# Kernel optimization log

Measured on AMD Instinct MI355X. Metric: run time of the kernel, lower is better.

## Reference

```python
import jax, jax.numpy as jnp
import numpy as np

D_MODEL = 256
NHEAD = 8
NUM_EXPERTS = 5
LQ, LK, BATCH = 100, 1024, 16
LN_EPS = 1e-5


def setup_inputs() -> dict:
    key = jax.random.key(0)
    ks = jax.random.split(key, 12)
    d, E = D_MODEL, NUM_EXPERTS
    s = 1.0 / np.sqrt(d)
    return {
        "tgt": jax.random.normal(ks[0], (LQ, BATCH, d), jnp.float32),
        "memory": jax.random.normal(ks[1], (LK, BATCH, d), jnp.float32),
        "query_pos": jax.random.normal(ks[2], (LQ, BATCH, d), jnp.float32),
        "pos": jax.random.normal(ks[3], (LK, BATCH, d), jnp.float32),
        # per-expert MultiheadAttention params (packed q,k,v in_proj like torch)
        "w_in": jax.random.normal(ks[4], (E, 3 * d, d), jnp.float32) * s,
        "b_in": jnp.zeros((E, 3 * d), jnp.float32),
        "w_out": jax.random.normal(ks[5], (E, d, d), jnp.float32) * s,
        "b_out": jnp.zeros((E, d), jnp.float32),
        # gating network
        "w_gate": jax.random.normal(ks[6], (E, d), jnp.float32) * s,
        "b_gate": jnp.zeros((E,), jnp.float32),
        # LayerNorm
        "ln_gamma": jnp.ones((d,), jnp.float32),
        "ln_beta": jnp.zeros((d,), jnp.float32),
    }


def _moe_cross_attn(tgt, memory, query_pos, pos, w_in, b_in, w_out, b_out,
                    w_gate, b_gate, ln_gamma, ln_beta):
    Lq, B, d = tgt.shape
    H = NHEAD
    hd = d // H
    E = w_in.shape[0]
    Lk = memory.shape[0]

    # gating over (seq*batch, d) -> softmax over experts
    gate = jax.nn.softmax(tgt @ w_gate.T + b_gate, axis=-1)  # (Lq, B, E)

    q_emb = tgt + query_pos      # (Lq, B, d)
    k_emb = memory + pos         # (Lk, B, d)

    wq, wk, wv = w_in[:, :d], w_in[:, d:2 * d], w_in[:, 2 * d:]
    bq, bk, bv = b_in[:, :d], b_in[:, d:2 * d], b_in[:, 2 * d:]

    # batched projections across all experts (replaces python loop of MHA calls)
    q = jnp.einsum('lbd,eod->elbo', q_emb, wq) + bq[:, None, None, :]
    k = jnp.einsum('sbd,eod->esbo', k_emb, wk) + bk[:, None, None, :]
    v = jnp.einsum('sbd,eod->esbo', memory, wv) + bv[:, None, None, :]

    q = q.reshape(E, Lq, B, H, hd) * (1.0 / np.sqrt(hd))
    k = k.reshape(E, Lk, B, H, hd)
    v = v.reshape(E, Lk, B, H, hd)

    scores = jnp.einsum('elbhk,esbhk->ebhls', q, k)      # (E, B, H, Lq, Lk)
    attn = jax.nn.softmax(scores, axis=-1)
    ctx = jnp.einsum('ebhls,esbhk->elbhk', attn, v).reshape(E, Lq, B, d)

    out = jnp.einsum('elbd,eod->elbo', ctx, w_out) + b_out[:, None, None, :]

    # softmax-gated weighted combine of expert outputs
    mo = jnp.einsum('lbe,elbd->lbd', gate, out)

    x = tgt + mo  # dropout is identity (p=0.0)
    mu = jnp.mean(x, axis=-1, keepdims=True)
    var = jnp.var(x, axis=-1, keepdims=True)
    return (x - mu) * jax.lax.rsqrt(var + LN_EPS) * ln_gamma + ln_beta


def reference(tgt, memory, query_pos, pos, w_in, b_in, w_out, b_out,
              w_gate, b_gate, ln_gamma, ln_beta):
    return _moe_cross_attn(tgt, memory, query_pos, pos, w_in, b_in, w_out,
                           b_out, w_gate, b_gate, ln_gamma, ln_beta)
```

## Files before the change

kernel.cpp:

```cpp
#include <hip/hip_runtime.h>


typedef __bf16 bf16x8 __attribute__((ext_vector_type(8)));
typedef float f32x4 __attribute__((ext_vector_type(4)));
typedef unsigned int u32x4 __attribute__((ext_vector_type(4)));
typedef unsigned int u32x2 __attribute__((ext_vector_type(2)));
typedef unsigned short u16x4 __attribute__((ext_vector_type(4)));
typedef unsigned short us;

__device__ __forceinline__ us f2bf(float f) {
    unsigned u = __builtin_bit_cast(unsigned, f);
    u += 0x7FFFu + ((u >> 16) & 1u);
    return (us)(u >> 16);
}

__device__ __forceinline__ float bf2f(us v) {
    unsigned u = ((unsigned)v) << 16;
    return __builtin_bit_cast(float, u);
}

__device__ __forceinline__ bf16x8 ld_bf8(const us* p) {
    return __builtin_bit_cast(bf16x8, *reinterpret_cast<const u32x4*>(p));
}

__device__ __forceinline__ void gld_lds16(const us* g, us* l) {
    __builtin_amdgcn_global_load_lds(
        (const __attribute__((address_space(1))) unsigned int*)g,
        (__attribute__((address_space(3))) unsigned int*)l, 16, 0, 0);
}

__launch_bounds__(256)
__global__ void cvt_all(const float* __restrict__ tgt, const float* __restrict__ qpos,
                        const float* __restrict__ mem, const float* __restrict__ pos,
                        const float* __restrict__ w_in, const float* __restrict__ w_out,
                        us* __restrict__ Aq, us* __restrict__ Ak, us* __restrict__ Av,
                        us* __restrict__ Wb, us* __restrict__ WOb)
{
    const int bid = blockIdx.x;
    const int tid = threadIdx.x;
    if (bid < 400) {
        int i = bid * 256 + tid;
        f32x4 a = reinterpret_cast<const f32x4*>(tgt)[i];
        f32x4 b = reinterpret_cast<const f32x4*>(qpos)[i];
        u16x4 r;
#pragma unroll
        for (int j = 0; j < 4; ++j) r[j] = f2bf(a[j] + b[j]);
        reinterpret_cast<u16x4*>(Aq)[i] = r;
    } else if (bid < 4496) {
        int i = (bid - 400) * 256 + tid;
        f32x4 m = reinterpret_cast<const f32x4*>(mem)[i];
        f32x4 p = reinterpret_cast<const f32x4*>(pos)[i];
        u16x4 rk, rv;
#pragma unroll
        for (int j = 0; j < 4; ++j) { rk[j] = f2bf(m[j] + p[j]); rv[j] = f2bf(m[j]); }
        reinterpret_cast<u16x4*>(Ak)[i] = rk;
        reinterpret_cast<u16x4*>(Av)[i] = rv;
    } else if (bid < 5456) {
        int i = (bid - 4496) * 256 + tid;
        f32x4 a = reinterpret_cast<const f32x4*>(w_in)[i];
        u16x4 r;
#pragma unroll
        for (int j = 0; j < 4; ++j) r[j] = f2bf(a[j]);
        reinterpret_cast<u16x4*>(Wb)[i] = r;
    } else {
        int i = (bid - 5456) * 256 + tid;
        f32x4 a = reinterpret_cast<const f32x4*>(w_out)[i];
        u16x4 r;
#pragma unroll
        for (int j = 0; j < 4; ++j) r[j] = f2bf(a[j]);
        reinterpret_cast<u16x4*>(WOb)[i] = r;
    }
}

template <bool BF16OUT>
__device__ __forceinline__ void gemm_body(const us* __restrict__ A,
                                          const us* __restrict__ W,
                                          const float* __restrict__ bias,
                                          void* __restrict__ Cout,
                                          float scale, int M)
{
    const int row0 = blockIdx.x * 128;
    const int col0 = blockIdx.y * 128;
    __shared__ us As[2 * 8192];
    __shared__ us Bs[2 * 8192];
    const int tid  = threadIdx.x;
    const int lane = tid & 63;
    const int w    = tid >> 6;
    const int l15  = lane & 15;
    const int quad = lane >> 4;
    const int wm   = (w >> 1) * 64;
    const int wn   = (w & 1) * 64;
    const int srow = lane >> 3;
    const int gofs = ((lane & 7) ^ srow) * 8;

#pragma unroll
    for (int cc = 0; cc < 4; ++cc) {
        const int c = w * 4 + cc;
        const int row = c * 8 + srow;
        gld_lds16(A + (size_t)(row0 + row) * 256 + gofs, &As[c * 512]);
        gld_lds16(W + (size_t)(col0 + row) * 256 + gofs, &Bs[c * 512]);
    }
    __syncthreads();

    f32x4 acc[4][4] = {};

#pragma unroll
    for (int kt = 0; kt < 4; ++kt) {
        const int cur = (kt & 1) * 8192;
        if (kt < 3) {
            const int nxt = ((kt + 1) & 1) * 8192;
            const int k0 = (kt + 1) * 64;
#pragma unroll
            for (int cc = 0; cc < 4; ++cc) {
                const int c = w * 4 + cc;
                const int row = c * 8 + srow;
                gld_lds16(A + (size_t)(row0 + row) * 256 + k0 + gofs, &As[nxt + c * 512]);
                gld_lds16(W + (size_t)(col0 + row) * 256 + k0 + gofs, &Bs[nxt + c * 512]);
            }
        }
#pragma unroll
        for (int kh = 0; kh < 2; ++kh) {
            bf16x8 af[4], bf[4];
#pragma unroll
            for (int mi = 0; mi < 4; ++mi) {
                const int row = wm + mi * 16 + l15;
                const int seg = (kh * 4 + quad) ^ (row & 7);
                af[mi] = ld_bf8(&As[cur + row * 64 + seg * 8]);
            }
#pragma unroll
            for (int ni = 0; ni < 4; ++ni) {
                const int col = wn + ni * 16 + l15;
                const int seg = (kh * 4 + quad) ^ (col & 7);
                bf[ni] = ld_bf8(&Bs[cur + col * 64 + seg * 8]);
            }
#pragma unroll
            for (int mi = 0; mi < 4; ++mi)
#pragma unroll
                for (int ni = 0; ni < 4; ++ni)
                    acc[mi][ni] = __builtin_amdgcn_mfma_f32_16x16x32_bf16(bf[ni], af[mi], acc[mi][ni], 0, 0, 0);
        }
        if (kt < 3) __syncthreads();
    }

#pragma unroll
    for (int ni = 0; ni < 4; ++ni) {
        const int colb = col0 + wn + ni * 16 + quad * 4;
        const f32x4 b4 = *reinterpret_cast<const f32x4*>(bias + colb);
#pragma unroll
        for (int mi = 0; mi < 4; ++mi) {
            const int row = row0 + wm + mi * 16 + l15;
            if (row < M) {
                if constexpr (BF16OUT) {
                    u32x2 pk;
                    pk[0] = (unsigned)f2bf((acc[mi][ni][0] + b4[0]) * scale)
                          | ((unsigned)f2bf((acc[mi][ni][1] + b4[1]) * scale) << 16);
                    pk[1] = (unsigned)f2bf((acc[mi][ni][2] + b4[2]) * scale)
                          | ((unsigned)f2bf((acc[mi][ni][3] + b4[3]) * scale) << 16);
                    *reinterpret_cast<u32x2*>(reinterpret_cast<us*>(Cout) + (size_t)row * 256 + colb) = pk;
                } else {
                    f32x4 v;
#pragma unroll
                    for (int r = 0; r < 4; ++r) v[r] = (acc[mi][ni][r] + b4[r]) * scale;
                    *reinterpret_cast<f32x4*>(reinterpret_cast<float*>(Cout) + (size_t)row * 256 + colb) = v;
                }
            }
        }
    }
}

__launch_bounds__(256)
__global__ void gemm_qkv(const us* __restrict__ Aq, const us* __restrict__ Ak,
                         const us* __restrict__ Av, const us* __restrict__ Wb,
                         const float* __restrict__ b_in,
                         us* __restrict__ Qb, us* __restrict__ Kb, us* __restrict__ Vb)
{
    const int z = blockIdx.z;
    if (z < 5) {
        if (blockIdx.x >= 13) return;
        gemm_body<true>(Aq, Wb + (size_t)z * 196608, b_in + (size_t)z * 768,
                        Qb + (size_t)z * 409600, 0.17677669529663687f, 1600);
    } else if (z < 10) {
        const int e = z - 5;
        gemm_body<true>(Ak, Wb + 65536 + (size_t)e * 196608, b_in + (size_t)e * 768 + 256,
                        Kb + (size_t)e * 4194304, 1.0f, 16384);
    } else {
        const int e = z - 10;
        gemm_body<true>(Av, Wb + 131072 + (size_t)e * 196608, b_in + (size_t)e * 768 + 512,
                        Vb + (size_t)e * 4194304, 1.0f, 16384);
    }
}

__launch_bounds__(256)
__global__ void gemm_o(const us* __restrict__ CTXb, const us* __restrict__ WOb,
                       const float* __restrict__ b_out, float* __restrict__ OUTf)
{
    const int e = blockIdx.z;
    gemm_body<false>(CTXb + (size_t)e * 409600, WOb + (size_t)e * 65536,
                     b_out + (size_t)e * 256, OUTf + (size_t)e * 409600, 1.0f, 1600);
}

__device__ __forceinline__ int vrow(int d) { return d * 264 + 8 * (d >> 3); }

__launch_bounds__(512)
__global__ void attn(const us* __restrict__ Qb, const us* __restrict__ Kb,
                     const us* __restrict__ Vb, us* __restrict__ PO,
                     float* __restrict__ PL)
{
    const int h = blockIdx.x;
    const int z = blockIdx.y;
    const int s = blockIdx.z;
    const int e = z >> 4, b = z & 15;
    const int tid  = threadIdx.x;
    const int w    = tid >> 6;
    const int lane = tid & 63;
    const int l15  = lane & 15, quad = lane >> 4;
    __shared__ us Ks[256 * 32];
    __shared__ us Vs[8464];
    __shared__ us Ps[7][16 * 40];

    const int key0 = s * 256;
    {
        const int kl  = lane >> 2;
        const int seg = lane & 3;
        const us* kg = Kb + ((size_t)((e * 1024 + key0 + w * 16 + kl) * 16 + b)) * 256
                          + h * 32 + seg * 8;
        gld_lds16(kg, &Ks[w * 512]);
        gld_lds16(kg + (size_t)128 * 16 * 256, &Ks[4096 + w * 512]);

        const int kv = tid >> 2;
        const int sg = tid & 3;
        const us* vg = Vb + ((size_t)((e * 1024 + key0 + kv) * 16 + b)) * 256
                          + h * 32 + sg * 8;
        u32x4 v0 = *reinterpret_cast<const u32x4*>(vg);
        u32x4 v1 = *reinterpret_cast<const u32x4*>(vg + (size_t)128 * 16 * 256);
#pragma unroll
        for (int j = 0; j < 4; ++j) {
            const int d0 = sg * 8 + 2 * j;
            const int e0 = vrow(d0);
            const int e1 = e0 + 264;
            Vs[e0 + kv]       = (us)(v0[j] & 0xffff);
            Vs[e1 + kv]       = (us)(v0[j] >> 16);
            Vs[e0 + 128 + kv] = (us)(v1[j] & 0xffff);
            Vs[e1 + 128 + kv] = (us)(v1[j] >> 16);
        }
    }
    u32x4 qraw = {0u, 0u, 0u, 0u};
    if (w < 7) {
        const int l = w * 16 + l15;
        if (l < 100)
            qraw = *reinterpret_cast<const u32x4*>(
                Qb + ((size_t)((e * 100 + l) * 16 + b)) * 256 + h * 32 + quad * 8);
    }
    const bf16x8 qf = __builtin_bit_cast(bf16x8, qraw);

    __syncthreads();

    if (w >= 7) return;

    const f32x4 zacc = {};
    f32x4 o0 = {}, o1 = {};
    float lsum = 0.0f;

    for (int c = 0; c < 8; ++c) {
        bf16x8 kf0 = ld_bf8(&Ks[(c * 32 + l15) * 32 + quad * 8]);
        bf16x8 kf1 = ld_bf8(&Ks[(c * 32 + 16 + l15) * 32 + quad * 8]);
        f32x4 s0 = __builtin_amdgcn_mfma_f32_16x16x32_bf16(kf0, qf, zacc, 0, 0, 0);
        f32x4 s1 = __builtin_amdgcn_mfma_f32_16x16x32_bf16(kf1, qf, zacc, 0, 0, 0);
        float p0[4], p1[4];
#pragma unroll
        for (int r = 0; r < 4; ++r) {
            p0[r] = __expf(s0[r]);
            p1[r] = __expf(s1[r]);
            lsum += p0[r] + p1[r];
        }
        u32x2 w0, w1;
        w0[0] = (unsigned)f2bf(p0[0]) | ((unsigned)f2bf(p0[1]) << 16);
        w0[1] = (unsigned)f2bf(p0[2]) | ((unsigned)f2bf(p0[3]) << 16);
        w1[0] = (unsigned)f2bf(p1[0]) | ((unsigned)f2bf(p1[1]) << 16);
        w1[1] = (unsigned)f2bf(p1[2]) | ((unsigned)f2bf(p1[3]) << 16);
        *reinterpret_cast<u32x2*>(&Ps[w][l15 * 40 + quad * 4])      = w0;
        *reinterpret_cast<u32x2*>(&Ps[w][l15 * 40 + 16 + quad * 4]) = w1;
        bf16x8 pf  = ld_bf8(&Ps[w][l15 * 40 + quad * 8]);
        bf16x8 vf0 = ld_bf8(&Vs[vrow(l15) + c * 32 + quad * 8]);
        bf16x8 vf1 = ld_bf8(&Vs[vrow(16 + l15) + c * 32 + quad * 8]);
        o0 = __builtin_amdgcn_mfma_f32_16x16x32_bf16(pf, vf0, o0, 0, 0, 0);
        o1 = __builtin_amdgcn_mfma_f32_16x16x32_bf16(pf, vf1, o1, 0, 0, 0);
    }

    lsum += __shfl_xor(lsum, 16, 64);
    lsum += __shfl_xor(lsum, 32, 64);

#pragma unroll
    for (int r = 0; r < 4; ++r) {
        const int row = w * 16 + quad * 4 + r;
        if (row < 100) {
            const size_t o = (((size_t)((s * 5 + e) * 100 + row)) * 16 + b) * 256 + h * 32;
            PO[o + l15]      = f2bf(o0[r]);
            PO[o + 16 + l15] = f2bf(o1[r]);
        }
    }
    const int q = w * 16 + l15;
    if (quad == 0 && q < 100)
        PL[((((size_t)s * 5 + e) * 16 + b) * 8 + h) * 128 + q] = lsum;
}

__launch_bounds__(256)
__global__ void combine(const us* __restrict__ PO, const float* __restrict__ PL,
                        us* __restrict__ CTX)
{
    const int blk = blockIdx.x;
    const int e   = blk / 1600;
    const int rem = blk - e * 1600;
    const int row = rem >> 4;
    const int b   = rem & 15;
    const int d   = threadIdx.x;
    const int h   = d >> 5;
    float O = 0.0f, L = 0.0f;
#pragma unroll
    for (int s = 0; s < 4; ++s) {
        O += bf2f(PO[(((size_t)((s * 5 + e) * 100 + row)) * 16 + b) * 256 + d]);
        L += PL[((((size_t)s * 5 + e) * 16 + b) * 8 + h) * 128 + row];
    }
    CTX[(((size_t)(e * 100 + row)) * 16 + b) * 256 + d] = f2bf(O / L);
}

__launch_bounds__(256)
__global__ void finalize(const float* __restrict__ tgt, const float* __restrict__ w_gate,
                         const float* __restrict__ b_gate, const float* __restrict__ OUTf,
                         const float* __restrict__ gamma, const float* __restrict__ beta,
                         float* __restrict__ out)
{
    const int row = blockIdx.x;
    const int d = threadIdx.x;
    __shared__ float red[4];
    const float t = tgt[(size_t)row * 256 + d];

    float g[5];
#pragma unroll
    for (int e = 0; e < 5; ++e) {
        float part = t * w_gate[e * 256 + d];
#pragma unroll
        for (int off = 32; off >= 1; off >>= 1) part += __shfl_xor(part, off, 64);
        if ((d & 63) == 0) red[d >> 6] = part;
        __syncthreads();
        g[e] = red[0] + red[1] + red[2] + red[3] + b_gate[e];
        __syncthreads();
    }
    float mx = g[0];
#pragma unroll
    for (int e = 1; e < 5; ++e) mx = fmaxf(mx, g[e]);
    float sm = 0.0f;
#pragma unroll
    for (int e = 0; e < 5; ++e) { g[e] = __expf(g[e] - mx); sm += g[e]; }
    const float invs = 1.0f / sm;

    float mo = 0.0f;
#pragma unroll
    for (int e = 0; e < 5; ++e)
        mo += g[e] * invs * OUTf[((size_t)e * 1600 + row) * 256 + d];
    const float x = t + mo;

    float part = x;
#pragma unroll
    for (int off = 32; off >= 1; off >>= 1) part += __shfl_xor(part, off, 64);
    if ((d & 63) == 0) red[d >> 6] = part;
    __syncthreads();
    const float mean = (red[0] + red[1] + red[2] + red[3]) * (1.0f / 256.0f);
    __syncthreads();

    const float diff = x - mean;
    part = diff * diff;
#pragma unroll
    for (int off = 32; off >= 1; off >>= 1) part += __shfl_xor(part, off, 64);
    if ((d & 63) == 0) red[d >> 6] = part;
    __syncthreads();
    const float var = (red[0] + red[1] + red[2] + red[3]) * (1.0f / 256.0f);

    out[(size_t)row * 256 + d] = diff * rsqrtf(var + 1e-5f) * gamma[d] + beta[d];
}

extern "C" void kernel_launch(void* const* d_in, const int* in_sizes, int n_in,
                              void* d_out, int out_size, void* d_ws, size_t ws_size,
                              hipStream_t stream)
{
    const float* tgt    = (const float*)d_in[0];
    const float* mem    = (const float*)d_in[1];
    const float* qpos   = (const float*)d_in[2];
    const float* pos    = (const float*)d_in[3];
    const float* w_in   = (const float*)d_in[4];
    const float* b_in   = (const float*)d_in[5];
    const float* w_out  = (const float*)d_in[6];
    const float* b_out  = (const float*)d_in[7];
    const float* w_gate = (const float*)d_in[8];
    const float* b_gate = (const float*)d_in[9];
    const float* ln_g   = (const float*)d_in[10];
    const float* ln_b   = (const float*)d_in[11];
    float* out = (float*)d_out;

    char* p = (char*)d_ws;
    auto alloc = [&](size_t n) { char* r = p; p += (n + 255) & ~(size_t)255; return r; };

    us* Aq   = (us*)alloc(409600ull * 2);
    us* Ak   = (us*)alloc(4194304ull * 2);
    us* Av   = (us*)alloc(4194304ull * 2);
    us* Wb   = (us*)alloc(983040ull * 2);
    us* WOb  = (us*)alloc(327680ull * 2);
    us* Qb   = (us*)alloc(5ull * 409600 * 2);
    us* Kb   = (us*)alloc(5ull * 4194304 * 2);
    us* Vb   = (us*)alloc(5ull * 4194304 * 2);
    us* CTXb = (us*)alloc(5ull * 409600 * 2);
    float* OUTf = (float*)alloc(5ull * 409600 * 4);
    us*    PO = (us*)d_ws;
    float* PL = (float*)((char*)d_ws + 16384000);

    cvt_all<<<5776, 256, 0, stream>>>(tgt, qpos, mem, pos, w_in, w_out,
                                      Aq, Ak, Av, Wb, WOb);

    gemm_qkv<<<dim3(128, 2, 15), 256, 0, stream>>>(Aq, Ak, Av, Wb, b_in, Qb, Kb, Vb);

    attn<<<dim3(8, 80, 4), 512, 0, stream>>>(Qb, Kb, Vb, PO, PL);

    combine<<<8000, 256, 0, stream>>>(PO, PL, CTXb);

    gemm_o<<<dim3(13, 2, 5), 256, 0, stream>>>(CTXb, WOb, b_out, OUTf);

    finalize<<<1600, 256, 0, stream>>>(tgt, w_gate, b_gate, OUTf, ln_g, ln_b, out);
}
```

Before: 214.5 us.

## Replace QKV projection GEMM with persistent weight-resident kernel

The QKV projection GEMM now runs as a persistent-style kernel of 260 blocks. Each block loads a 128x256 weight slice into LDS once, then streams 64-row A tiles through a double buffer across a range of row tiles, writing bf16 output with the bias added. This avoids reloading weights for every 128x128 output tile and drops the early-exit blocks of the old 3D grid. In exchange each block holds a large LDS footprint, which limits occupancy, and work is split statically across a fixed number of blocks. The gemm_o epilogue loop order is also swapped.

Measured after the change: 247.8 us. 1.16x slower.

```diff
diff --git a/kernel.cpp b/kernel.cpp
--- a/kernel.cpp
+++ b/kernel.cpp
@@ -69,6 +69,129 @@
 #pragma unroll
         for (int j = 0; j < 4; ++j) r[j] = f2bf(a[j]);
         reinterpret_cast<u16x4*>(WOb)[i] = r;
+    }
+}
+
+__launch_bounds__(256)
+__global__ void gemm_qkv_p(const us* __restrict__ Aq, const us* __restrict__ Ak,
+                           const us* __restrict__ Av, const us* __restrict__ Wb,
+                           const float* __restrict__ b_in,
+                           us* __restrict__ Qb, us* __restrict__ Kb, us* __restrict__ Vb)
+{
+    __shared__ us Ws[128 * 256];
+    __shared__ us Asb[2][64 * 64];
+    const int tid  = threadIdx.x;
+    const int lane = tid & 63;
+    const int w    = tid >> 6;
+    const int l15  = lane & 15;
+    const int quad = lane >> 4;
+
+    const int bid = blockIdx.x;
+    const us* A; us* Cout; const float* bias; float scale; int t0, t1;
+    const us* Wg;
+    if (bid < 240) {
+        const int c = bid / 12, sub = bid % 12;
+        const int e = c >> 2, mh = c & 3;
+        const int mat = (mh >> 1) + 1;
+        const int half = mh & 1;
+        A     = (mat == 1) ? Ak : Av;
+        Wg    = Wb + (size_t)e * 196608 + mat * 65536 + half * 32768;
+        bias  = b_in + e * 768 + mat * 256 + half * 128;
+        Cout  = ((mat == 1) ? Kb : Vb) + (size_t)e * 4194304 + half * 128;
+        scale = 1.0f;
+        t0 = sub * 22; t1 = min(256, t0 + 22);
+    } else {
+        const int q = bid - 240;
+        const int c = q >> 1, sub = q & 1;
+        const int e = c >> 1, half = c & 1;
+        A     = Aq;
+        Wg    = Wb + (size_t)e * 196608 + half * 32768;
+        bias  = b_in + e * 768 + half * 128;
+        Cout  = Qb + (size_t)e * 409600 + half * 128;
+        scale = 0.17677669529663687f;
+        t0 = sub * 13; t1 = min(25, t0 + 13);
+    }
+
+#pragma unroll
+    for (int k = 0; k < 16; ++k) {
+        const int flat = k * 256 + tid;
+        const int row = flat >> 5, s = flat & 31;
+        const int gs = (s & 24) | ((s & 7) ^ (row & 7));
+        gld_lds16(Wg + (size_t)row * 256 + gs * 8, &Ws[flat * 8]);
+    }
+
+    const int srow = lane >> 3;
+    const int aseg = lane & 7;
+    auto stageA = [&](int buf, int t, int kt) {
+#pragma unroll
+        for (int cc = 0; cc < 2; ++cc) {
+            const int c = w + cc * 4;
+            const int row = c * 8 + srow;
+            const int gs = aseg ^ srow;
+            gld_lds16(A + (size_t)(t * 64 + row) * 256 + kt * 64 + gs * 8,
+                      &Asb[buf][c * 512 + lane * 8]);
+        }
+    };
+
+    stageA(0, t0, 0);
+    __syncthreads();
+
+    f32x4 acc[4][2];
+    const int total = (t1 - t0) * 4;
+    int buf = 0;
+    for (int it = 0; it < total; ++it) {
+        const int t  = t0 + (it >> 2);
+        const int kt = it & 3;
+        if (it + 1 < total)
+            stageA(buf ^ 1, t0 + ((it + 1) >> 2), (it + 1) & 3);
+        if (kt == 0) {
+#pragma unroll
+            for (int mi = 0; mi < 4; ++mi)
+#pragma unroll
+                for (int ni = 0; ni < 2; ++ni) acc[mi][ni] = f32x4{};
+        }
+#pragma unroll
+        for (int kh = 0; kh < 2; ++kh) {
+            bf16x8 af[4], bf[2];
+#pragma unroll
+            for (int mi = 0; mi < 4; ++mi) {
+                const int row = mi * 16 + l15;
+                const int seg = (kh * 4 + quad) ^ (row & 7);
+                af[mi] = ld_bf8(&Asb[buf][row * 64 + seg * 8]);
+            }
+#pragma unroll
+            for (int ni = 0; ni < 2; ++ni) {
+                const int col = w * 32 + ni * 16 + l15;
+                const int seg = kt * 8 + kh * 4 + quad;
+                const int sw = (seg & 24) | ((seg & 7) ^ (col & 7));
+                bf[ni] = ld_bf8(&Ws[col * 256 + sw * 8]);
+            }
+#pragma unroll
+            for (int mi = 0; mi < 4; ++mi)
+#pragma unroll
+                for (int ni = 0; ni < 2; ++ni)
+                    acc[mi][ni] = __builtin_amdgcn_mfma_f32_16x16x32_bf16(bf[ni], af[mi], acc[mi][ni], 0, 0, 0);
+        }
+        if (kt == 3) {
+#pragma unroll
+            for (int mi = 0; mi < 4; ++mi) {
+                const int row = t * 64 + mi * 16 + l15;
+                us* cp = Cout + (size_t)row * 256;
+#pragma unroll
+                for (int ni = 0; ni < 2; ++ni) {
+                    const int colb = w * 32 + ni * 16 + quad * 4;
+                    const f32x4 b4 = *reinterpret_cast<const f32x4*>(bias + colb);
+                    u32x2 pk;
+                    pk[0] = (unsigned)f2bf((acc[mi][ni][0] + b4[0]) * scale)
+                          | ((unsigned)f2bf((acc[mi][ni][1] + b4[1]) * scale) << 16);
+                    pk[1] = (unsigned)f2bf((acc[mi][ni][2] + b4[2]) * scale)
+                          | ((unsigned)f2bf((acc[mi][ni][3] + b4[3]) * scale) << 16);
+                    *reinterpret_cast<u32x2*>(cp + colb) = pk;
+                }
+            }
+        }
+        __syncthreads();
+        buf ^= 1;
     }
 }
 
@@ -143,11 +266,11 @@
     }
 
 #pragma unroll
-    for (int ni = 0; ni < 4; ++ni) {
-        const int colb = col0 + wn + ni * 16 + quad * 4;
-        const f32x4 b4 = *reinterpret_cast<const f32x4*>(bias + colb);
-#pragma unroll
-        for (int mi = 0; mi < 4; ++mi) {
+    for (int mi = 0; mi < 4; ++mi) {
+#pragma unroll
+        for (int ni = 0; ni < 4; ++ni) {
+            const int colb = col0 + wn + ni * 16 + quad * 4;
+            const f32x4 b4 = *reinterpret_cast<const f32x4*>(bias + colb);
             const int row = row0 + wm + mi * 16 + l15;
             if (row < M) {
                 if constexpr (BF16OUT) {
@@ -165,28 +288,6 @@
                 }
             }
         }
-    }
-}
-
-__launch_bounds__(256)
-__global__ void gemm_qkv(const us* __restrict__ Aq, const us* __restrict__ Ak,
-                         const us* __restrict__ Av, const us* __restrict__ Wb,
-                         const float* __restrict__ b_in,
-                         us* __restrict__ Qb, us* __restrict__ Kb, us* __restrict__ Vb)
-{
-    const int z = blockIdx.z;
-    if (z < 5) {
-        if (blockIdx.x >= 13) return;
-        gemm_body<true>(Aq, Wb + (size_t)z * 196608, b_in + (size_t)z * 768,
-                        Qb + (size_t)z * 409600, 0.17677669529663687f, 1600);
-    } else if (z < 10) {
-        const int e = z - 5;
-        gemm_body<true>(Ak, Wb + 65536 + (size_t)e * 196608, b_in + (size_t)e * 768 + 256,
-                        Kb + (size_t)e * 4194304, 1.0f, 16384);
-    } else {
-        const int e = z - 10;
-        gemm_body<true>(Av, Wb + 131072 + (size_t)e * 196608, b_in + (size_t)e * 768 + 512,
-                        Vb + (size_t)e * 4194304, 1.0f, 16384);
     }
 }
 
@@ -416,7 +517,7 @@
     cvt_all<<<5776, 256, 0, stream>>>(tgt, qpos, mem, pos, w_in, w_out,
                                       Aq, Ak, Av, Wb, WOb);
 
-    gemm_qkv<<<dim3(128, 2, 15), 256, 0, stream>>>(Aq, Ak, Av, Wb, b_in, Qb, Kb, Vb);
+    gemm_qkv_p<<<260, 256, 0, stream>>>(Aq, Ak, Av, Wb, b_in, Qb, Kb, Vb);
 
     attn<<<dim3(8, 80, 4), 512, 0, stream>>>(Qb, Kb, Vb, PO, PL);
 
```

## Fuse activation fp32-to-bf16 conversion and pos add into QKV GEMM A-loads

Applied to the files above, without the earlier changes.

Removes the separate conversion pass over tgt/memory/pos and instead loads fp32 activations directly inside the QKV GEMM. The pos add and bf16 pack happen in registers before the LDS store. Global loads for the next k-tile are issued ahead of the MFMA loop to overlap latency. This avoids writing and re-reading roughly 17 MB of bf16 intermediates. In exchange, the GEMM reads twice as many fp32 bytes per K tile and uses more registers, with launch bounds now requesting 2 blocks per CU. PO/PL also move to dedicated workspace instead of aliasing the freed buffers.

Result: slower. 263.6 us (+22.9%).

```diff
diff --git a/kernel.cpp b/kernel.cpp
--- a/kernel.cpp
+++ b/kernel.cpp
@@ -14,6 +14,10 @@
     return (us)(u >> 16);
 }
 
+__device__ __forceinline__ unsigned pack2(float lo, float hi) {
+    return (unsigned)f2bf(lo) | ((unsigned)f2bf(hi) << 16);
+}
+
 __device__ __forceinline__ float bf2f(us v) {
     unsigned u = ((unsigned)v) << 16;
     return __builtin_bit_cast(float, u);
@@ -30,40 +34,20 @@
 }
 
 __launch_bounds__(256)
-__global__ void cvt_all(const float* __restrict__ tgt, const float* __restrict__ qpos,
-                        const float* __restrict__ mem, const float* __restrict__ pos,
-                        const float* __restrict__ w_in, const float* __restrict__ w_out,
-                        us* __restrict__ Aq, us* __restrict__ Ak, us* __restrict__ Av,
-                        us* __restrict__ Wb, us* __restrict__ WOb)
+__global__ void cvt_w(const float* __restrict__ w_in, const float* __restrict__ w_out,
+                      us* __restrict__ Wb, us* __restrict__ WOb)
 {
     const int bid = blockIdx.x;
     const int tid = threadIdx.x;
-    if (bid < 400) {
+    if (bid < 960) {
         int i = bid * 256 + tid;
-        f32x4 a = reinterpret_cast<const f32x4*>(tgt)[i];
-        f32x4 b = reinterpret_cast<const f32x4*>(qpos)[i];
-        u16x4 r;
-#pragma unroll
-        for (int j = 0; j < 4; ++j) r[j] = f2bf(a[j] + b[j]);
-        reinterpret_cast<u16x4*>(Aq)[i] = r;
-    } else if (bid < 4496) {
-        int i = (bid - 400) * 256 + tid;
-        f32x4 m = reinterpret_cast<const f32x4*>(mem)[i];
-        f32x4 p = reinterpret_cast<const f32x4*>(pos)[i];
-        u16x4 rk, rv;
-#pragma unroll
-        for (int j = 0; j < 4; ++j) { rk[j] = f2bf(m[j] + p[j]); rv[j] = f2bf(m[j]); }
-        reinterpret_cast<u16x4*>(Ak)[i] = rk;
-        reinterpret_cast<u16x4*>(Av)[i] = rv;
-    } else if (bid < 5456) {
-        int i = (bid - 4496) * 256 + tid;
         f32x4 a = reinterpret_cast<const f32x4*>(w_in)[i];
         u16x4 r;
 #pragma unroll
         for (int j = 0; j < 4; ++j) r[j] = f2bf(a[j]);
         reinterpret_cast<u16x4*>(Wb)[i] = r;
     } else {
-        int i = (bid - 5456) * 256 + tid;
+        int i = (bid - 960) * 256 + tid;
         f32x4 a = reinterpret_cast<const f32x4*>(w_out)[i];
         u16x4 r;
 #pragma unroll
@@ -72,12 +56,11 @@
     }
 }
 
-template <bool BF16OUT>
-__device__ __forceinline__ void gemm_body(const us* __restrict__ A,
-                                          const us* __restrict__ W,
-                                          const float* __restrict__ bias,
-                                          void* __restrict__ Cout,
-                                          float scale, int M)
+template <bool TWO>
+__device__ __forceinline__ void gemm_f32_body(
+    const float* __restrict__ a1, const float* __restrict__ a2,
+    const us* __restrict__ Wg, const float* __restrict__ bias,
+    us* __restrict__ Cout, float scale, int M)
 {
     const int row0 = blockIdx.x * 128;
     const int col0 = blockIdx.y * 128;
@@ -93,6 +76,158 @@
     const int srow = lane >> 3;
     const int gofs = ((lane & 7) ^ srow) * 8;
 
+    f32x4 P[4][2], Q2[4][2];
+
+    auto loadA = [&](int kt) {
+#pragma unroll
+        for (int cc = 0; cc < 4; ++cc) {
+            const int c = w * 4 + cc;
+            const int row = c * 8 + srow;
+            const int gr = (row0 + row < M) ? (row0 + row) : (M - 1);
+            const float* p = a1 + (size_t)gr * 256 + kt * 64 + gofs;
+            P[cc][0] = *reinterpret_cast<const f32x4*>(p);
+            P[cc][1] = *reinterpret_cast<const f32x4*>(p + 4);
+            if constexpr (TWO) {
+                const float* q = a2 + (size_t)gr * 256 + kt * 64 + gofs;
+                Q2[cc][0] = *reinterpret_cast<const f32x4*>(q);
+                Q2[cc][1] = *reinterpret_cast<const f32x4*>(q + 4);
+            }
+        }
+    };
+    auto writeA = [&](int buf) {
+#pragma unroll
+        for (int cc = 0; cc < 4; ++cc) {
+            const int c = w * 4 + cc;
+            f32x4 e0 = P[cc][0], e1 = P[cc][1];
+            if constexpr (TWO) { e0 += Q2[cc][0]; e1 += Q2[cc][1]; }
+            u32x4 pk;
+            pk[0] = pack2(e0[0], e0[1]);
+            pk[1] = pack2(e0[2], e0[3]);
+            pk[2] = pack2(e1[0], e1[1]);
+            pk[3] = pack2(e1[2], e1[3]);
+            *reinterpret_cast<u32x4*>(&As[buf * 8192 + c * 512 + lane * 8]) = pk;
+        }
+    };
+    auto loadW = [&](int buf, int kt) {
+#pragma unroll
+        for (int cc = 0; cc < 4; ++cc) {
+            const int c = w * 4 + cc;
+            const int row = c * 8 + srow;
+            gld_lds16(Wg + (size_t)(col0 + row) * 256 + kt * 64 + gofs,
+                      &Bs[buf * 8192 + c * 512]);
+        }
+    };
+
+    loadA(0);
+    loadW(0, 0);
+    writeA(0);
+    __syncthreads();
+
+    f32x4 acc[4][4] = {};
+
+#pragma unroll
+    for (int kt = 0; kt < 4; ++kt) {
+        const int cur = kt & 1;
+        if (kt < 3) {
+            loadA(kt + 1);
+            loadW(cur ^ 1, kt + 1);
+        }
+#pragma unroll
+        for (int kh = 0; kh < 2; ++kh) {
+            bf16x8 af[4], bf[4];
+#pragma unroll
+            for (int mi = 0; mi < 4; ++mi) {
+                const int row = wm + mi * 16 + l15;
+                const int seg = (kh * 4 + quad) ^ (row & 7);
+                af[mi] = ld_bf8(&As[cur * 8192 + row * 64 + seg * 8]);
+            }
+#pragma unroll
+            for (int ni = 0; ni < 4; ++ni) {
+                const int col = wn + ni * 16 + l15;
+                const int seg = (kh * 4 + quad) ^ (col & 7);
+                bf[ni] = ld_bf8(&Bs[cur * 8192 + col * 64 + seg * 8]);
+            }
+#pragma unroll
+            for (int mi = 0; mi < 4; ++mi)
+#pragma unroll
+                for (int ni = 0; ni < 4; ++ni)
+                    acc[mi][ni] = __builtin_amdgcn_mfma_f32_16x16x32_bf16(bf[ni], af[mi], acc[mi][ni], 0, 0, 0);
+        }
+        if (kt < 3) {
+            writeA(cur ^ 1);
+            __syncthreads();
+        }
+    }
+
+#pragma unroll
+    for (int mi = 0; mi < 4; ++mi) {
+        const int row = row0 + wm + mi * 16 + l15;
+        if (row < M) {
+            us* cp = Cout + (size_t)row * 256;
+#pragma unroll
+            for (int ni = 0; ni < 4; ++ni) {
+                const int colb = col0 + wn + ni * 16 + quad * 4;
+                const f32x4 b4 = *reinterpret_cast<const f32x4*>(bias + colb);
+                u32x2 pk;
+                pk[0] = pack2((acc[mi][ni][0] + b4[0]) * scale,
+                              (acc[mi][ni][1] + b4[1]) * scale);
+                pk[1] = pack2((acc[mi][ni][2] + b4[2]) * scale,
+                              (acc[mi][ni][3] + b4[3]) * scale);
+                *reinterpret_cast<u32x2*>(cp + colb) = pk;
+            }
+        }
+    }
+}
+
+__launch_bounds__(256, 2)
+__global__ void gemm_qkv(const float* __restrict__ tgt, const float* __restrict__ qpos,
+                         const float* __restrict__ mem, const float* __restrict__ pos,
+                         const us* __restrict__ Wb, const float* __restrict__ b_in,
+                         us* __restrict__ Qb, us* __restrict__ Kb, us* __restrict__ Vb)
+{
+    const int z = blockIdx.z;
+    if (z < 5) {
+        if (blockIdx.x >= 13) return;
+        gemm_f32_body<true>(tgt, qpos, Wb + (size_t)z * 196608, b_in + (size_t)z * 768,
+                            Qb + (size_t)z * 409600, 0.17677669529663687f, 1600);
+    } else if (z < 10) {
+        const int e = z - 5;
+        gemm_f32_body<true>(mem, pos, Wb + 65536 + (size_t)e * 196608,
+                            b_in + (size_t)e * 768 + 256,
+                            Kb + (size_t)e * 4194304, 1.0f, 16384);
+    } else {
+        const int e = z - 10;
+        gemm_f32_body<false>(mem, nullptr, Wb + 131072 + (size_t)e * 196608,
+                             b_in + (size_t)e * 768 + 512,
+                             Vb + (size_t)e * 4194304, 1.0f, 16384);
+    }
+}
+
+__launch_bounds__(256)
+__global__ void gemm_o(const us* __restrict__ CTXall, const us* __restrict__ WOall,
+                       const float* __restrict__ b_out, float* __restrict__ OUTall)
+{
+    const int e = blockIdx.z;
+    const us* A = CTXall + (size_t)e * 409600;
+    const us* W = WOall + (size_t)e * 65536;
+    const float* bias = b_out + (size_t)e * 256;
+    float* Cout = OUTall + (size_t)e * 409600;
+    const int M = 1600;
+
+    const int row0 = blockIdx.x * 128;
+    const int col0 = blockIdx.y * 128;
+    __shared__ us As[2 * 8192];
+    __shared__ us Bs[2 * 8192];
+    const int tid  = threadIdx.x;
+    const int lane = tid & 63;
+    const int w    = tid >> 6;
+    const int l15  = lane & 15;
+    const int quad = lane >> 4;
+    const int wm   = (w >> 1) * 64;
+    const int wn   = (w & 1) * 64;
+    const int srow = lane >> 3;
+    const int gofs = ((lane & 7) ^ srow) * 8;
+
 #pragma unroll
     for (int cc = 0; cc < 4; ++cc) {
         const int c = w * 4 + cc;
@@ -143,60 +278,20 @@
     }
 
 #pragma unroll
-    for (int ni = 0; ni < 4; ++ni) {
-        const int colb = col0 + wn + ni * 16 + quad * 4;
-        const f32x4 b4 = *reinterpret_cast<const f32x4*>(bias + colb);
-#pragma unroll
-        for (int mi = 0; mi < 4; ++mi) {
-            const int row = row0 + wm + mi * 16 + l15;
-            if (row < M) {
-                if constexpr (BF16OUT) {
-                    u32x2 pk;
-                    pk[0] = (unsigned)f2bf((acc[mi][ni][0] + b4[0]) * scale)
-                          | ((unsigned)f2bf((acc[mi][ni][1] + b4[1]) * scale) << 16);
-                    pk[1] = (unsigned)f2bf((acc[mi][ni][2] + b4[2]) * scale)
-                          | ((unsigned)f2bf((acc[mi][ni][3] + b4[3]) * scale) << 16);
-                    *reinterpret_cast<u32x2*>(reinterpret_cast<us*>(Cout) + (size_t)row * 256 + colb) = pk;
-                } else {
-                    f32x4 v;
-#pragma unroll
-                    for (int r = 0; r < 4; ++r) v[r] = (acc[mi][ni][r] + b4[r]) * scale;
-                    *reinterpret_cast<f32x4*>(reinterpret_cast<float*>(Cout) + (size_t)row * 256 + colb) = v;
-                }
-            }
-        }
-    }
-}
-
-__launch_bounds__(256)
-__global__ void gemm_qkv(const us* __restrict__ Aq, const us* __restrict__ Ak,
-                         const us* __restrict__ Av, const us* __restrict__ Wb,
-                         const float* __restrict__ b_in,
-                         us* __restrict__ Qb, us* __restrict__ Kb, us* __restrict__ Vb)
-{
-    const int z = blockIdx.z;
-    if (z < 5) {
-        if (blockIdx.x >= 13) return;
-        gemm_body<true>(Aq, Wb + (size_t)z * 196608, b_in + (size_t)z * 768,
-                        Qb + (size_t)z * 409600, 0.17677669529663687f, 1600);
-    } else if (z < 10) {
-        const int e = z - 5;
-        gemm_body<true>(Ak, Wb + 65536 + (size_t)e * 196608, b_in + (size_t)e * 768 + 256,
-                        Kb + (size_t)e * 4194304, 1.0f, 16384);
-    } else {
-        const int e = z - 10;
-        gemm_body<true>(Av, Wb + 131072 + (size_t)e * 196608, b_in + (size_t)e * 768 + 512,
-                        Vb + (size_t)e * 4194304, 1.0f, 16384);
-    }
-}
-
-__launch_bounds__(256)
-__global__ void gemm_o(const us* __restrict__ CTXb, const us* __restrict__ WOb,
-                       const float* __restrict__ b_out, float* __restrict__ OUTf)
-{
-    const int e = blockIdx.z;
-    gemm_body<false>(CTXb + (size_t)e * 409600, WOb + (size_t)e * 65536,
-                     b_out + (size_t)e * 256, OUTf + (size_t)e * 409600, 1.0f, 1600);
+    for (int mi = 0; mi < 4; ++mi) {
+        const int row = row0 + wm + mi * 16 + l15;
+        if (row < M) {
+#pragma unroll
+            for (int ni = 0; ni < 4; ++ni) {
+                const int colb = col0 + wn + ni * 16 + quad * 4;
+                const f32x4 b4 = *reinterpret_cast<const f32x4*>(bias + colb);
+                f32x4 v;
+#pragma unroll
+                for (int r = 0; r < 4; ++r) v[r] = acc[mi][ni][r] + b4[r];
+                *reinterpret_cast<f32x4*>(Cout + (size_t)row * 256 + colb) = v;
+            }
+        }
+    }
 }
 
 __device__ __forceinline__ int vrow(int d) { return d * 264 + 8 * (d >> 3); }
@@ -274,10 +369,10 @@
             lsum += p0[r] + p1[r];
         }
         u32x2 w0, w1;
-        w0[0] = (unsigned)f2bf(p0[0]) | ((unsigned)f2bf(p0[1]) << 16);
-        w0[1] = (unsigned)f2bf(p0[2]) | ((unsigned)f2bf(p0[3]) << 16);
-        w1[0] = (unsigned)f2bf(p1[0]) | ((unsigned)f2bf(p1[1]) << 16);
-        w1[1] = (unsigned)f2bf(p1[2]) | ((unsigned)f2bf(p1[3]) << 16);
+        w0[0] = pack2(p0[0], p0[1]);
+        w0[1] = pack2(p0[2], p0[3]);
+        w1[0] = pack2(p1[0], p1[1]);
+        w1[1] = pack2(p1[2], p1[3]);
         *reinterpret_cast<u32x2*>(&Ps[w][l15 * 40 + quad * 4])      = w0;
         *reinterpret_cast<u32x2*>(&Ps[w][l15 * 40 + 16 + quad * 4]) = w1;
         bf16x8 pf  = ld_bf8(&Ps[w][l15 * 40 + quad * 8]);
@@ -400,9 +495,6 @@
     char* p = (char*)d_ws;
     auto alloc = [&](size_t n) { char* r = p; p += (n + 255) & ~(size_t)255; return r; };
 
-    us* Aq   = (us*)alloc(409600ull * 2);
-    us* Ak   = (us*)alloc(4194304ull * 2);
-    us* Av   = (us*)alloc(4194304ull * 2);
     us* Wb   = (us*)alloc(983040ull * 2);
     us* WOb  = (us*)alloc(327680ull * 2);
     us* Qb   = (us*)alloc(5ull * 409600 * 2);
@@ -410,13 +502,13 @@
     us* Vb   = (us*)alloc(5ull * 4194304 * 2);
     us* CTXb = (us*)alloc(5ull * 409600 * 2);
     float* OUTf = (float*)alloc(5ull * 409600 * 4);
-    us*    PO = (us*)d_ws;
-    float* PL = (float*)((char*)d_ws + 16384000);
-
-    cvt_all<<<5776, 256, 0, stream>>>(tgt, qpos, mem, pos, w_in, w_out,
-                                      Aq, Ak, Av, Wb, WOb);
-
-    gemm_qkv<<<dim3(128, 2, 15), 256, 0, stream>>>(Aq, Ak, Av, Wb, b_in, Qb, Kb, Vb);
+    us*    PO = (us*)alloc(4ull * 5 * 409600 * 2);
+    float* PL = (float*)alloc(4ull * 5 * 16 * 8 * 128 * 4);
+
+    cvt_w<<<1280, 256, 0, stream>>>(w_in, w_out, Wb, WOb);
+
+    gemm_qkv<<<dim3(128, 2, 15), 256, 0, stream>>>(
+        tgt, qpos, mem, pos, Wb, b_in, Qb, Kb, Vb);
 
     attn<<<dim3(8, 80, 4), 512, 0, stream>>>(Qb, Kb, Vb, PO, PL);
 
```
